# Optimization experiments

Measured on AMD Instinct MI355X. Metric: run time of the kernel, lower is better.

Reference implementation:

```python
import jax, jax.numpy as jnp
import numpy as np

DIM = 256
HEADS = 8
WIN = (8, 8)
DQ = 4   # num_frames_q
DKV = 4  # num_frames_kv
N1 = DQ * WIN[0] * WIN[1]   # 256
N2 = DKV * WIN[0] * WIN[1]  # 256
B_ = 256   # B * nW
NW = 128   # windows per batch element


def _rel_pos_index():
    # mirrors WindowAttention3D.__init__ (torch.meshgrid default indexing='ij')
    coords_d_q = np.arange(DQ)
    step = (DQ + 1) // DKV
    if step != 0:
        coords_d_kv = np.arange(0, DQ, step)
    else:
        coords_d_kv = np.zeros(DKV, dtype=np.int64)
    ch = np.arange(WIN[0])
    cw = np.arange(WIN[1])
    cq = np.stack(np.meshgrid(coords_d_q, ch, cw, indexing='ij'))   # (3, DQ, Wh, Ww)
    ckv = np.stack(np.meshgrid(coords_d_kv, ch, cw, indexing='ij'))
    qf = cq.reshape(3, -1)   # (3, N1)
    kf = ckv.reshape(3, -1)  # (3, N2)
    rel = (qf[:, :, None] - kf[:, None, :]).transpose(1, 2, 0)  # (N1, N2, 3)
    rel[..., 0] += DQ - 1
    rel[..., 1] += WIN[0] - 1
    rel[..., 2] += WIN[1] - 1
    rel[..., 0] *= (2 * WIN[0] - 1) * (2 * WIN[1] - 1)
    rel[..., 1] *= 2 * WIN[1] - 1
    return rel.sum(-1)  # (N1, N2)


def setup_inputs() -> dict:
    key = jax.random.key(0)
    ks = jax.random.split(key, 10)
    table_sz = (2 * DQ - 1) * (2 * WIN[0] - 1) * (2 * WIN[1] - 1)  # 1575
    inp = {
        'q': jax.random.normal(ks[0], (B_, N1, DIM), jnp.float32),
        'kv': jax.random.normal(ks[1], (B_, N2, DIM), jnp.float32),
        'mask': jax.random.normal(ks[2], (NW, N1, N2), jnp.float32),
        'Wq': jax.random.normal(ks[3], (DIM, DIM), jnp.float32) * 0.02,
        'bq': jnp.zeros((DIM,), jnp.float32),
        'Wkv': jax.random.normal(ks[4], (2 * DIM, DIM), jnp.float32) * 0.02,
        'bkv': jnp.zeros((2 * DIM,), jnp.float32),
        'bias_table': jax.random.normal(ks[5], (table_sz, HEADS), jnp.float32) * 0.02,
        'Wp': jax.random.normal(ks[6], (DIM, DIM), jnp.float32) * 0.02,
        'bp': jnp.zeros((DIM,), jnp.float32),
        'rel_index': jnp.asarray(_rel_pos_index(), jnp.int32),
    }
    return inp


def reference(q, kv, mask, Wq, bq, Wkv, bkv, bias_table, Wp, bp, rel_index):
    B, n1, C = q.shape
    n2 = kv.shape[1]
    hd = C // HEADS
    scale = hd ** -0.5
    # projections
    qh = (q @ Wq.T + bq).reshape(B, n1, HEADS, hd).transpose(0, 2, 1, 3)      # (B,H,N1,hd)
    kvh = (kv @ Wkv.T + bkv).reshape(B, n2, 2, HEADS, hd).transpose(2, 0, 3, 1, 4)
    k, v = kvh[0], kvh[1]                                                      # (B,H,N2,hd)
    attn = jnp.einsum('bhqd,bhkd->bhqk', qh * scale, k)                        # (B,H,N1,N2)
    # relative position bias gather
    bias = bias_table[rel_index]                                               # (N1,N2,H)
    attn = attn + bias.transpose(2, 0, 1)[None]
    # shift mask (nW, N1, N2) broadcast over batch and heads
    nW = mask.shape[0]
    attn = attn.reshape(B // nW, nW, HEADS, n1, n2) + mask[None, :, None]
    attn = jax.nn.softmax(attn.reshape(B, HEADS, n1, n2), axis=-1)
    x = jnp.einsum('bhqk,bhkd->bqhd', attn, v).reshape(B, n1, C)
    x = x @ Wp.T + bp
    return x
```

## Files before the change

### kernel.cpp

```cpp
#include <hip/hip_runtime.h>
#include <type_traits>

#define BH_TOTAL 2048
#define SCALE_Q 0.17677669529663687f

typedef unsigned short ushort;
typedef unsigned int uint;
typedef __attribute__((ext_vector_type(8))) short bf16x8;
typedef __attribute__((ext_vector_type(4))) ushort u16x4;
typedef __attribute__((ext_vector_type(4))) float f32x4;

static __device__ __forceinline__ ushort f2bf(float f) {
    union { float f; uint u; } v; v.f = f;
    uint r = (v.u + 0x7fffu + ((v.u >> 16) & 1u)) >> 16;
    return (ushort)r;
}
static __device__ __forceinline__ ushort bfru(float f) {
    union { float f; uint u; } v; v.f = f;
    return (ushort)((v.u + 0x8000u) >> 16);
}
static __device__ __forceinline__ float bflo(uint w) {
    union { uint u; float f; } v; v.u = w << 16; return v.f;
}
static __device__ __forceinline__ float bfhi(uint w) {
    union { uint u; float f; } v; v.u = w & 0xffff0000u; return v.f;
}

__global__ __launch_bounds__(256)
void mask_pre(const float* __restrict__ mask, ushort* __restrict__ maskP)
{
    __shared__ float row[256];
    const int wr = blockIdx.x;
    const int tid = threadIdx.x;
    row[tid] = mask[(size_t)wr * 256 + tid];
    __syncthreads();
    maskP[(size_t)wr * 256 + tid] = f2bf(row[(tid & 15) * 16 + (tid >> 4)]);
}

__global__ __launch_bounds__(256)
void bias_pre(const float* __restrict__ bias_table, const int* __restrict__ rel_index,
              ushort* __restrict__ biasP)
{
    __shared__ float row[256];
    const int hr = blockIdx.x;
    const int h = hr >> 8, r = hr & 255;
    const int tid = threadIdx.x;
    row[tid] = bias_table[rel_index[r * 256 + tid] * 8 + h];
    __syncthreads();
    biasP[(size_t)hr * 256 + tid] = f2bf(row[(tid & 15) * 16 + (tid >> 4)]);
}

template<int MODE, typename AT>
__global__ __launch_bounds__(256)
void gemm_mfma(const AT* __restrict__ A, const float* __restrict__ W,
               const float* __restrict__ bias, float* __restrict__ outf,
               ushort* __restrict__ outh0, ushort* __restrict__ outh1)
{
    __shared__ ushort As[128 * 72];
    __shared__ ushort Bs[128 * 72];

    const int tid  = threadIdx.x;
    const int m0   = blockIdx.x * 128;
    const int n0   = blockIdx.y * 128;
    const int lane = tid & 63, wave = tid >> 6;
    const int col  = lane & 15, quad = lane >> 4;
    const int wm   = (wave >> 1) * 64, wn = (wave & 1) * 64;

    f32x4 acc[4][4];
    #pragma unroll
    for (int i = 0; i < 4; ++i)
        #pragma unroll
        for (int j = 0; j < 4; ++j)
            acc[i][j] = (f32x4){0.f, 0.f, 0.f, 0.f};

    for (int k0 = 0; k0 < 256; k0 += 64) {
        __syncthreads();
        if constexpr (std::is_same<AT, float>::value) {
            #pragma unroll
            for (int i = 0; i < 8; ++i) {
                int f = tid + 256 * i;
                int row = f >> 4, c4 = f & 15;
                float4 av = *(const float4*)&A[(size_t)(m0 + row) * 256 + k0 + c4 * 4];
                u16x4 p = {bfru(av.x), bfru(av.y), bfru(av.z), bfru(av.w)};
                *(u16x4*)&As[row * 72 + c4 * 4] = p;
            }
        } else {
            #pragma unroll
            for (int i = 0; i < 4; ++i) {
                int f = tid + 256 * i;
                int row = f >> 3, c8 = f & 7;
                *(bf16x8*)&As[row * 72 + c8 * 8] =
                    *(const bf16x8*)&A[(size_t)(m0 + row) * 256 + k0 + c8 * 8];
            }
        }
        #pragma unroll
        for (int i = 0; i < 8; ++i) {
            int f = tid + 256 * i;
            int row = f >> 4, c4 = f & 15;
            float4 wv = *(const float4*)&W[(size_t)(n0 + row) * 256 + k0 + c4 * 4];
            u16x4 p = {bfru(wv.x), bfru(wv.y), bfru(wv.z), bfru(wv.w)};
            *(u16x4*)&Bs[row * 72 + c4 * 4] = p;
        }
        __syncthreads();
        #pragma unroll
        for (int ks = 0; ks < 64; ks += 32) {
            bf16x8 af[4], bfr[4];
            #pragma unroll
            for (int t = 0; t < 4; ++t) {
                af[t]  = *(const bf16x8*)&As[(wm + t * 16 + col) * 72 + ks + quad * 8];
                bfr[t] = *(const bf16x8*)&Bs[(wn + t * 16 + col) * 72 + ks + quad * 8];
            }
            #pragma unroll
            for (int mt = 0; mt < 4; ++mt)
                #pragma unroll
                for (int nt = 0; nt < 4; ++nt)
                    acc[mt][nt] = __builtin_amdgcn_mfma_f32_16x16x32_bf16(
                        af[mt], bfr[nt], acc[mt][nt], 0, 0, 0);
        }
    }

    #pragma unroll
    for (int mt = 0; mt < 4; ++mt) {
        const int mb = m0 + wm + mt * 16 + quad * 4;
        #pragma unroll
        for (int nt = 0; nt < 4; ++nt) {
            const int n = n0 + wn + nt * 16 + col;
            const float bn = bias[n];
            if (MODE == 1 && n >= 256) {
                const int nn = n - 256;
                const int b = mb >> 8, m1 = mb & 255;
                u16x4 p;
                #pragma unroll
                for (int r = 0; r < 4; ++r)
                    p[r] = f2bf(acc[mt][nt][r] + bn);
                *(u16x4*)&outh1[(size_t)((b << 3) | (nn >> 5)) * 8192
                                + (nn & 31) * 256 + m1] = p;
            } else {
                #pragma unroll
                for (int r = 0; r < 4; ++r) {
                    int m = mb + r;
                    int b = m >> 8, m1 = m & 255;
                    float v = acc[mt][nt][r] + bn;
                    if (MODE == 0) {
                        outh0[(size_t)((b << 3) | (n >> 5)) * 8192 + m1 * 32 + (n & 31)]
                            = f2bf(v * SCALE_Q);
                    } else if (MODE == 1) {
                        outh0[(size_t)((b << 3) | (n >> 5)) * 8192 + m1 * 32 + (n & 31)]
                            = f2bf(v);
                    } else {
                        outf[(size_t)m * 256 + n] = v;
                    }
                }
            }
        }
    }
}

__global__ __launch_bounds__(256)
void attn_mfma(const ushort* __restrict__ qh, const ushort* __restrict__ kb,
               const ushort* __restrict__ vt, const ushort* __restrict__ maskP,
               const ushort* __restrict__ biasP, ushort* __restrict__ xbuf)
{
    __shared__ ushort Ks[256 * 40];
    __shared__ ushort Vts[32 * 264];
    __shared__ ushort Ps[4][16 * 264];

    const int bh   = blockIdx.x;
    const int b    = bh >> 3, h = bh & 7;
    const int tid  = threadIdx.x;
    const int lane = tid & 63, wave = tid >> 6;
    const int col  = lane & 15;
    const int quad = lane >> 4;

    const ushort* __restrict__ Qg  = qh + (size_t)bh * 8192;
    const ushort* __restrict__ Kg  = kb + (size_t)bh * 8192;
    const ushort* __restrict__ Vg  = vt + (size_t)bh * 8192;
    const ushort* __restrict__ MgP = maskP + (size_t)(b & 127) * 65536;
    const ushort* __restrict__ BgP = biasP + (size_t)h * 65536;

    for (int t = tid; t < 1024; t += 256) {
        int j = t >> 2, p = t & 3;
        *(bf16x8*)&Ks[j * 40 + p * 8] = *(const bf16x8*)&Kg[j * 32 + p * 8];
    }
    for (int t = tid; t < 1024; t += 256) {
        int d = t >> 5, p = t & 31;
        *(bf16x8*)&Vts[d * 264 + p * 8] = *(const bf16x8*)&Vg[d * 256 + p * 8];
    }
    __syncthreads();

    ushort* __restrict__ Pw = &Ps[wave][0];
    const f32x4 zero = {0.f, 0.f, 0.f, 0.f};

    for (int it = 0; it < 4; ++it) {
        const int q0 = (wave * 4 + it) * 16;

        uint4 mA[4], mB[4], bA[4], bB[4];
        #pragma unroll
        for (int r = 0; r < 4; ++r) {
            const ushort* mp = &MgP[((q0 + quad * 4 + r) * 16 + col) * 16];
            const ushort* bp = &BgP[((q0 + quad * 4 + r) * 16 + col) * 16];
            mA[r] = *(const uint4*)mp;  mB[r] = *(const uint4*)(mp + 8);
            bA[r] = *(const uint4*)bp;  bB[r] = *(const uint4*)(bp + 8);
        }

        bf16x8 aq = *(const bf16x8*)&Qg[(q0 + col) * 32 + quad * 8];
        f32x4 acc[16];
        #pragma unroll
        for (int jt = 0; jt < 16; ++jt) {
            bf16x8 bk = *(const bf16x8*)&Ks[(jt * 16 + col) * 40 + quad * 8];
            acc[jt] = __builtin_amdgcn_mfma_f32_16x16x32_bf16(aq, bk, zero, 0, 0, 0);
        }

        #pragma unroll
        for (int r = 0; r < 4; ++r) {
            uint mw[8] = {mA[r].x, mA[r].y, mA[r].z, mA[r].w,
                          mB[r].x, mB[r].y, mB[r].z, mB[r].w};
            uint bw[8] = {bA[r].x, bA[r].y, bA[r].z, bA[r].w,
                          bB[r].x, bB[r].y, bB[r].z, bB[r].w};
            #pragma unroll
            for (int jt = 0; jt < 16; ++jt) {
                float mv = (jt & 1) ? bfhi(mw[jt >> 1]) : bflo(mw[jt >> 1]);
                float bv = (jt & 1) ? bfhi(bw[jt >> 1]) : bflo(bw[jt >> 1]);
                acc[jt][r] += mv + bv;
            }
        }

        float mx[4], sm[4], inv[4];
        #pragma unroll
        for (int r = 0; r < 4; ++r) {
            float m = acc[0][r];
            #pragma unroll
            for (int jt = 1; jt < 16; ++jt) m = fmaxf(m, acc[jt][r]);
            #pragma unroll
            for (int off = 1; off < 16; off <<= 1) m = fmaxf(m, __shfl_xor(m, off));
            mx[r] = m;
            sm[r] = 0.f;
        }
        #pragma unroll
        for (int jt = 0; jt < 16; ++jt) {
            #pragma unroll
            for (int r = 0; r < 4; ++r) {
                float e = __expf(acc[jt][r] - mx[r]);
                acc[jt][r] = e;
                sm[r] += e;
            }
        }
        #pragma unroll
        for (int r = 0; r < 4; ++r) {
            float s = sm[r];
            #pragma unroll
            for (int off = 1; off < 16; off <<= 1) s += __shfl_xor(s, off);
            inv[r] = 1.0f / s;
        }

        #pragma unroll
        for (int jt = 0; jt < 16; ++jt) {
            #pragma unroll
            for (int r = 0; r < 4; ++r)
                Pw[(quad * 4 + r) * 264 + jt * 16 + col] = f2bf(acc[jt][r]);
        }

        f32x4 x0 = zero, x1 = zero;
        #pragma unroll
        for (int kc = 0; kc < 8; ++kc) {
            bf16x8 ap  = *(const bf16x8*)&Pw[col * 264 + kc * 32 + quad * 8];
            bf16x8 bv0 = *(const bf16x8*)&Vts[col * 264 + kc * 32 + quad * 8];
            bf16x8 bv1 = *(const bf16x8*)&Vts[(col + 16) * 264 + kc * 32 + quad * 8];
            x0 = __builtin_amdgcn_mfma_f32_16x16x32_bf16(ap, bv0, x0, 0, 0, 0);
            x1 = __builtin_amdgcn_mfma_f32_16x16x32_bf16(ap, bv1, x1, 0, 0, 0);
        }

        #pragma unroll
        for (int r = 0; r < 4; ++r) {
            int row = q0 + quad * 4 + r;
            size_t base = (size_t)(b * 256 + row) * 256 + h * 32;
            xbuf[base + col]      = f2bf(x0[r] * inv[r]);
            xbuf[base + 16 + col] = f2bf(x1[r] * inv[r]);
        }
    }
}

extern "C" void kernel_launch(void* const* d_in, const int* in_sizes, int n_in,
                              void* d_out, int out_size, void* d_ws, size_t ws_size,
                              hipStream_t stream)
{
    const float* q          = (const float*)d_in[0];
    const float* kv         = (const float*)d_in[1];
    const float* mask       = (const float*)d_in[2];
    const float* Wq         = (const float*)d_in[3];
    const float* bq         = (const float*)d_in[4];
    const float* Wkv        = (const float*)d_in[5];
    const float* bkv        = (const float*)d_in[6];
    const float* bias_table = (const float*)d_in[7];
    const float* Wp         = (const float*)d_in[8];
    const float* bp         = (const float*)d_in[9];
    const int*   rel_index  = (const int*)d_in[10];
    float* out = (float*)d_out;

    char* ws = (char*)d_ws;
    ushort* qhb = (ushort*)(ws);
    ushort* kbb = (ushort*)(ws + (size_t)33554432);
    ushort* vtb = (ushort*)(ws + (size_t)67108864);
    ushort* xb  = (ushort*)(ws + (size_t)100663296);
    ushort* mP  = (ushort*)(ws + (size_t)134217728);
    ushort* bP  = (ushort*)(ws + (size_t)150994944);

    dim3 blk(256);
    mask_pre<<<dim3(32768), blk, 0, stream>>>(mask, mP);
    bias_pre<<<dim3(2048),  blk, 0, stream>>>(bias_table, rel_index, bP);
    gemm_mfma<0, float ><<<dim3(512, 2), blk, 0, stream>>>(q,  Wq,  bq,  nullptr, qhb, nullptr);
    gemm_mfma<1, float ><<<dim3(512, 4), blk, 0, stream>>>(kv, Wkv, bkv, nullptr, kbb, vtb);
    attn_mfma<<<dim3(BH_TOTAL), blk, 0, stream>>>(qhb, kbb, vtb, mP, bP, xb);
    gemm_mfma<2, ushort><<<dim3(512, 2), blk, 0, stream>>>(xb, Wp, bp, out, nullptr, nullptr);
}
```

Before: 417.9 us.

## Pre-convert inputs to bf16, repack mask/bias, and feed bias into MFMA accumulator

New measurement: 432.2 us. 1.03x slower.

```diff
diff --git a/kernel.cpp b/kernel.cpp
--- a/kernel.cpp
+++ b/kernel.cpp
@@ -1,5 +1,4 @@
 #include <hip/hip_runtime.h>
-#include <type_traits>
 
 #define BH_TOTAL 2048
 #define SCALE_Q 0.17677669529663687f
@@ -27,32 +26,67 @@
 }
 
 __global__ __launch_bounds__(256)
+void cvt_all(const float* __restrict__ q, const float* __restrict__ kv,
+             const float* __restrict__ Wq, const float* __restrict__ Wkv,
+             const float* __restrict__ Wp,
+             ushort* __restrict__ qb, ushort* __restrict__ kvb,
+             ushort* __restrict__ wqb, ushort* __restrict__ wkvb,
+             ushort* __restrict__ wpb)
+{
+    const int bid = blockIdx.x, tid = threadIdx.x;
+    const float* src; ushort* dst; int base;
+    if (bid < 8192)       { src = q;   dst = qb;   base = bid; }
+    else if (bid < 16384) { src = kv;  dst = kvb;  base = bid - 8192; }
+    else if (bid < 16416) { src = Wq;  dst = wqb;  base = bid - 16384; }
+    else if (bid < 16480) { src = Wkv; dst = wkvb; base = bid - 16416; }
+    else                  { src = Wp;  dst = wpb;  base = bid - 16480; }
+    size_t off = ((size_t)base * 256 + tid) * 8;
+    float4 a = *(const float4*)&src[off];
+    float4 b = *(const float4*)&src[off + 4];
+    bf16x8 p = {(short)f2bf(a.x), (short)f2bf(a.y), (short)f2bf(a.z), (short)f2bf(a.w),
+                (short)f2bf(b.x), (short)f2bf(b.y), (short)f2bf(b.z), (short)f2bf(b.w)};
+    *(bf16x8*)&dst[off] = p;
+}
+
+__global__ __launch_bounds__(256)
 void mask_pre(const float* __restrict__ mask, ushort* __restrict__ maskP)
 {
-    __shared__ float row[256];
-    const int wr = blockIdx.x;
+    __shared__ float rows[1024];
+    const int w = blockIdx.x >> 6, qb = blockIdx.x & 63;
     const int tid = threadIdx.x;
-    row[tid] = mask[(size_t)wr * 256 + tid];
+    const float* src = mask + (size_t)w * 65536 + qb * 1024;
+    #pragma unroll
+    for (int i = 0; i < 4; ++i) rows[tid + 256 * i] = src[tid + 256 * i];
     __syncthreads();
-    maskP[(size_t)wr * 256 + tid] = f2bf(row[(tid & 15) * 16 + (tid >> 4)]);
+    const int jt = tid & 15, col = tid >> 4;
+    u16x4 p;
+    #pragma unroll
+    for (int r = 0; r < 4; ++r) p[r] = f2bf(rows[r * 256 + jt * 16 + col]);
+    *(u16x4*)&maskP[(size_t)w * 65536 + qb * 1024 + tid * 4] = p;
 }
 
 __global__ __launch_bounds__(256)
 void bias_pre(const float* __restrict__ bias_table, const int* __restrict__ rel_index,
-              ushort* __restrict__ biasP)
-{
-    __shared__ float row[256];
-    const int hr = blockIdx.x;
-    const int h = hr >> 8, r = hr & 255;
+              float* __restrict__ biasF)
+{
+    __shared__ int idx[1024];
+    const int h = blockIdx.x >> 6, qb = blockIdx.x & 63;
     const int tid = threadIdx.x;
-    row[tid] = bias_table[rel_index[r * 256 + tid] * 8 + h];
+    const int* src = rel_index + qb * 1024;
+    #pragma unroll
+    for (int i = 0; i < 4; ++i) idx[tid + 256 * i] = src[tid + 256 * i];
     __syncthreads();
-    biasP[(size_t)hr * 256 + tid] = f2bf(row[(tid & 15) * 16 + (tid >> 4)]);
-}
-
-template<int MODE, typename AT>
-__global__ __launch_bounds__(256)
-void gemm_mfma(const AT* __restrict__ A, const float* __restrict__ W,
+    const int jt = tid & 15, col = tid >> 4;
+    f32x4 p;
+    #pragma unroll
+    for (int r = 0; r < 4; ++r)
+        p[r] = bias_table[idx[r * 256 + jt * 16 + col] * 8 + h];
+    *(f32x4*)&biasF[(size_t)h * 65536 + qb * 1024 + tid * 4] = p;
+}
+
+template<int MODE>
+__global__ __launch_bounds__(256)
+void gemm_mfma(const ushort* __restrict__ A, const ushort* __restrict__ W,
                const float* __restrict__ bias, float* __restrict__ outf,
                ushort* __restrict__ outh0, ushort* __restrict__ outh1)
 {
@@ -60,8 +94,8 @@
     __shared__ ushort Bs[128 * 72];
 
     const int tid  = threadIdx.x;
-    const int m0   = blockIdx.x * 128;
-    const int n0   = blockIdx.y * 128;
+    const int n0   = blockIdx.x * 128;
+    const int m0   = blockIdx.y * 128;
     const int lane = tid & 63, wave = tid >> 6;
     const int col  = lane & 15, quad = lane >> 4;
     const int wm   = (wave >> 1) * 64, wn = (wave & 1) * 64;
@@ -75,31 +109,19 @@
 
     for (int k0 = 0; k0 < 256; k0 += 64) {
         __syncthreads();
-        if constexpr (std::is_same<AT, float>::value) {
-            #pragma unroll
-            for (int i = 0; i < 8; ++i) {
-                int f = tid + 256 * i;
-                int row = f >> 4, c4 = f & 15;
-                float4 av = *(const float4*)&A[(size_t)(m0 + row) * 256 + k0 + c4 * 4];
-                u16x4 p = {bfru(av.x), bfru(av.y), bfru(av.z), bfru(av.w)};
-                *(u16x4*)&As[row * 72 + c4 * 4] = p;
-            }
-        } else {
-            #pragma unroll
-            for (int i = 0; i < 4; ++i) {
-                int f = tid + 256 * i;
-                int row = f >> 3, c8 = f & 7;
-                *(bf16x8*)&As[row * 72 + c8 * 8] =
-                    *(const bf16x8*)&A[(size_t)(m0 + row) * 256 + k0 + c8 * 8];
-            }
-        }
-        #pragma unroll
-        for (int i = 0; i < 8; ++i) {
+        #pragma unroll
+        for (int i = 0; i < 4; ++i) {
             int f = tid + 256 * i;
-            int row = f >> 4, c4 = f & 15;
-            float4 wv = *(const float4*)&W[(size_t)(n0 + row) * 256 + k0 + c4 * 4];
-            u16x4 p = {bfru(wv.x), bfru(wv.y), bfru(wv.z), bfru(wv.w)};
-            *(u16x4*)&Bs[row * 72 + c4 * 4] = p;
+            int row = f >> 3, c8 = f & 7;
+            *(bf16x8*)&As[row * 72 + c8 * 8] =
+                *(const bf16x8*)&A[(size_t)(m0 + row) * 256 + k0 + c8 * 8];
+        }
+        #pragma unroll
+        for (int i = 0; i < 4; ++i) {
+            int f = tid + 256 * i;
+            int row = f >> 3, c8 = f & 7;
+            *(bf16x8*)&Bs[row * 72 + c8 * 8] =
+                *(const bf16x8*)&W[(size_t)(n0 + row) * 256 + k0 + c8 * 8];
         }
         __syncthreads();
         #pragma unroll
@@ -159,14 +181,18 @@
 __global__ __launch_bounds__(256)
 void attn_mfma(const ushort* __restrict__ qh, const ushort* __restrict__ kb,
                const ushort* __restrict__ vt, const ushort* __restrict__ maskP,
-               const ushort* __restrict__ biasP, ushort* __restrict__ xbuf)
+               const float* __restrict__ biasF, ushort* __restrict__ xbuf)
 {
     __shared__ ushort Ks[256 * 40];
     __shared__ ushort Vts[32 * 264];
     __shared__ ushort Ps[4][16 * 264];
 
-    const int bh   = blockIdx.x;
-    const int b    = bh >> 3, h = bh & 7;
+    const int g  = blockIdx.x;
+    const int w  = g >> 4;
+    const int b2 = (g >> 3) & 1, h = g & 7;
+    const int b  = b2 * 128 + w;
+    const int bh = b * 8 + h;
+
     const int tid  = threadIdx.x;
     const int lane = tid & 63, wave = tid >> 6;
     const int col  = lane & 15;
@@ -175,8 +201,8 @@
     const ushort* __restrict__ Qg  = qh + (size_t)bh * 8192;
     const ushort* __restrict__ Kg  = kb + (size_t)bh * 8192;
     const ushort* __restrict__ Vg  = vt + (size_t)bh * 8192;
-    const ushort* __restrict__ MgP = maskP + (size_t)(b & 127) * 65536;
-    const ushort* __restrict__ BgP = biasP + (size_t)h * 65536;
+    const ushort* __restrict__ MgP = maskP + (size_t)w * 65536;
+    const float*  __restrict__ BgF = biasF + (size_t)h * 65536;
 
     for (int t = tid; t < 1024; t += 256) {
         int j = t >> 2, p = t & 3;
@@ -193,36 +219,29 @@
 
     for (int it = 0; it < 4; ++it) {
         const int q0 = (wave * 4 + it) * 16;
-
-        uint4 mA[4], mB[4], bA[4], bB[4];
-        #pragma unroll
-        for (int r = 0; r < 4; ++r) {
-            const ushort* mp = &MgP[((q0 + quad * 4 + r) * 16 + col) * 16];
-            const ushort* bp = &BgP[((q0 + quad * 4 + r) * 16 + col) * 16];
-            mA[r] = *(const uint4*)mp;  mB[r] = *(const uint4*)(mp + 8);
-            bA[r] = *(const uint4*)bp;  bB[r] = *(const uint4*)(bp + 8);
-        }
+        const int qb = (q0 >> 2) + quad;
+
+        const ushort* mp  = &MgP[(size_t)(qb * 16 + col) * 64];
+        const float*  bp2 = &BgF[(size_t)(qb * 16 + col) * 64];
+        uint4 mq[8];
+        #pragma unroll
+        for (int i = 0; i < 8; ++i) mq[i] = *(const uint4*)&mp[i * 8];
 
         bf16x8 aq = *(const bf16x8*)&Qg[(q0 + col) * 32 + quad * 8];
         f32x4 acc[16];
         #pragma unroll
         for (int jt = 0; jt < 16; ++jt) {
+            f32x4 bv = *(const f32x4*)&bp2[jt * 4];
+            uint u0, u1;
+            if (jt & 1) { u0 = mq[jt >> 1].z; u1 = mq[jt >> 1].w; }
+            else        { u0 = mq[jt >> 1].x; u1 = mq[jt >> 1].y; }
+            f32x4 c;
+            c[0] = bv[0] + bflo(u0);
+            c[1] = bv[1] + bfhi(u0);
+            c[2] = bv[2] + bflo(u1);
+            c[3] = bv[3] + bfhi(u1);
             bf16x8 bk = *(const bf16x8*)&Ks[(jt * 16 + col) * 40 + quad * 8];
-            acc[jt] = __builtin_amdgcn_mfma_f32_16x16x32_bf16(aq, bk, zero, 0, 0, 0);
-        }
-
-        #pragma unroll
-        for (int r = 0; r < 4; ++r) {
-            uint mw[8] = {mA[r].x, mA[r].y, mA[r].z, mA[r].w,
-                          mB[r].x, mB[r].y, mB[r].z, mB[r].w};
-            uint bw[8] = {bA[r].x, bA[r].y, bA[r].z, bA[r].w,
-                          bB[r].x, bB[r].y, bB[r].z, bB[r].w};
-            #pragma unroll
-            for (int jt = 0; jt < 16; ++jt) {
-                float mv = (jt & 1) ? bfhi(mw[jt >> 1]) : bflo(mw[jt >> 1]);
-                float bv = (jt & 1) ? bfhi(bw[jt >> 1]) : bflo(bw[jt >> 1]);
-                acc[jt][r] += mv + bv;
-            }
+            acc[jt] = __builtin_amdgcn_mfma_f32_16x16x32_bf16(aq, bk, c, 0, 0, 0);
         }
 
         float mx[4], sm[4], inv[4];
@@ -257,7 +276,7 @@
         for (int jt = 0; jt < 16; ++jt) {
             #pragma unroll
             for (int r = 0; r < 4; ++r)
-                Pw[(quad * 4 + r) * 264 + jt * 16 + col] = f2bf(acc[jt][r]);
+                Pw[(quad * 4 + r) * 264 + jt * 16 + col] = bfru(acc[jt][r]);
         }
 
         f32x4 x0 = zero, x1 = zero;
@@ -298,18 +317,25 @@
     float* out = (float*)d_out;
 
     char* ws = (char*)d_ws;
-    ushort* qhb = (ushort*)(ws);
-    ushort* kbb = (ushort*)(ws + (size_t)33554432);
-    ushort* vtb = (ushort*)(ws + (size_t)67108864);
-    ushort* xb  = (ushort*)(ws + (size_t)100663296);
-    ushort* mP  = (ushort*)(ws + (size_t)134217728);
-    ushort* bP  = (ushort*)(ws + (size_t)150994944);
+    ushort* qhb   = (ushort*)(ws);
+    ushort* qb16  = (ushort*)(ws + (size_t)33554432);
+    ushort* kbb   = (ushort*)(ws + (size_t)33554432);
+    ushort* vtb   = (ushort*)(ws + (size_t)67108864);
+    ushort* kvb16 = (ushort*)(ws + (size_t)100663296);
+    ushort* xb    = (ushort*)(ws + (size_t)100663296);
+    ushort* mP    = (ushort*)(ws + (size_t)134217728);
+    float*  bF    = (float*) (ws + (size_t)150994944);
+    ushort* wqb   = (ushort*)(ws + (size_t)153092096);
+    ushort* wkvb  = (ushort*)(ws + (size_t)153223168);
+    ushort* wpb   = (ushort*)(ws + (size_t)153485312);
 
     dim3 blk(256);
-    mask_pre<<<dim3(32768), blk, 0, stream>>>(mask, mP);
-    bias_pre<<<dim3(2048),  blk, 0, stream>>>(bias_table, rel_index, bP);
-    gemm_mfma<0, float ><<<dim3(512, 2), blk, 0, stream>>>(q,  Wq,  bq,  nullptr, qhb, nullptr);
-    gemm_mfma<1, float ><<<dim3(512, 4), blk, 0, stream>>>(kv, Wkv, bkv, nullptr, kbb, vtb);
-    attn_mfma<<<dim3(BH_TOTAL), blk, 0, stream>>>(qhb, kbb, vtb, mP, bP, xb);
-    gemm_mfma<2, ushort><<<dim3(512, 2), blk, 0, stream>>>(xb, Wp, bp, out, nullptr, nullptr);
-}
+    cvt_all<<<dim3(16512), blk, 0, stream>>>(q, kv, Wq, Wkv, Wp,
+                                             qb16, kvb16, wqb, wkvb, wpb);
+    mask_pre<<<dim3(8192), blk, 0, stream>>>(mask, mP);
+    bias_pre<<<dim3(512),  blk, 0, stream>>>(bias_table, rel_index, bF);
+    gemm_mfma<0><<<dim3(2, 512), blk, 0, stream>>>(qb16,  wqb,  bq,  nullptr, qhb, nullptr);
+    gemm_mfma<1><<<dim3(4, 512), blk, 0, stream>>>(kvb16, wkvb, bkv, nullptr, kbb, vtb);
+    attn_mfma<<<dim3(BH_TOTAL), blk, 0, stream>>>(qhb, kbb, vtb, mP, bF, xb);
+    gemm_mfma<2><<<dim3(2, 512), blk, 0, stream>>>(xb, wpb, bp, out, nullptr, nullptr);
+}
```
